# Optimization experiments

Hardware: AMD Instinct MI355X
Metric: run time of the kernel (lower is better)

The kernel has to match this reference:

```python
import jax, jax.numpy as jnp
import numpy as np

GRID_SIZE = 5
SPLINE_ORDER = 3
GRID_RANGE = (-0.2, 0.2)
N_TOK, IN_CH, OUT_CH = 8192, 1024, 1024
K_COEF = GRID_SIZE + SPLINE_ORDER  # 8 basis functions per feature


def _make_grid():
    lo, hi = GRID_RANGE
    h = (hi - lo) / GRID_SIZE
    # 12 knots, extended by spline_order on both sides
    return (jnp.arange(-SPLINE_ORDER, GRID_SIZE + SPLINE_ORDER + 1, dtype=jnp.float32) * h + lo)


def _b_splines(x, grid):
    # x: [N, in] -> bases: [N, in, K_COEF] via Cox-de Boor recursion
    xe = x[..., None]                      # [N, in, 1]
    G = grid.shape[0]                      # 12
    bases = ((xe >= grid[:-1]) & (xe < grid[1:])).astype(x.dtype)  # [N, in, G-1]
    for k in range(1, SPLINE_ORDER + 1):
        left = (xe - grid[: G - k - 1]) / (grid[k : G - 1] - grid[: G - k - 1]) * bases[..., :-1]
        right = (grid[k + 1 :] - xe) / (grid[k + 1 :] - grid[1 : G - k]) * bases[..., 1:]
        bases = left + right
    return bases                            # [N, in, 8]


def _kan_layer(x, base_w, spline_w, grid):
    # base_activation = Identity
    base_out = x @ base_w.T                               # [N, out]
    bases = _b_splines(x, grid)                           # [N, in, K]
    spline_out = jnp.einsum('nik,oik->no', bases, spline_w)
    return base_out + spline_out


def setup_inputs() -> dict:
    key = jax.random.key(0)
    k1, k2, k3, k4, k5 = jax.random.split(key, 5)
    lo, hi = GRID_RANGE
    x = jax.random.uniform(k1, (N_TOK, IN_CH), dtype=jnp.float32, minval=lo, maxval=hi)
    s = 0.1 / np.sqrt(IN_CH)
    return {
        'x': x,
        'base_w1': jax.random.normal(k2, (OUT_CH, IN_CH), dtype=jnp.float32) * s,
        'spline_w1': jax.random.normal(k3, (OUT_CH, IN_CH, K_COEF), dtype=jnp.float32) * s,
        'base_w2': jax.random.normal(k4, (OUT_CH, OUT_CH), dtype=jnp.float32) * s,
        'spline_w2': jax.random.normal(k5, (OUT_CH, OUT_CH, K_COEF), dtype=jnp.float32) * s,
    }


def reference(x, base_w1, spline_w1, base_w2, spline_w2):
    grid = _make_grid()
    x1 = _kan_layer(x, base_w1, spline_w1, grid)
    x2 = _kan_layer(x1, base_w2, spline_w2, grid)
    return x2
```

## Files before the change

kernel.cpp:

```cpp
#include <hip/hip_runtime.h>
#include <hip/hip_bf16.h>

typedef __attribute__((ext_vector_type(8))) short bf16x8;
typedef __attribute__((ext_vector_type(4))) float f32x4;
typedef __attribute__((ext_vector_type(4))) unsigned int u32x4;

#define KCAT 9216
#define NTOK 8192
#define CH   1024
#define KHALF 4608
#define BK   64
#define NT   (KHALF / BK)
#define NH   (2 * NT)

__device__ __forceinline__ unsigned short f2bf(float f) {
    union { float f; unsigned int u; } v; v.f = f;
    unsigned int r = v.u + 0x7fffu + ((v.u >> 16) & 1u);
    return (unsigned short)(r >> 16);
}

__device__ __forceinline__ void load16_to_lds(const void* gp, void* lp) {
    __builtin_amdgcn_global_load_lds(
        (__attribute__((address_space(1))) void*)(void*)gp,
        (__attribute__((address_space(3))) void*)lp,
        16, 0, 0);
}

__device__ __forceinline__ void bases8_cf(float x, unsigned int* w) {
    float p  = (x + 0.44f) * 12.5f;
    float mf = floorf(p);
    float u  = p - mf;
    int   m  = (int)mf;
    float v  = 1.0f - u;
    float u2 = u * u, u3 = u2 * u;
    float N0 = v * v * v * (1.0f / 6.0f);
    float N1 = 0.5f * u3 - u2 + (2.0f / 3.0f);
    float N3 = u3 * (1.0f / 6.0f);
    float N2 = 1.0f - N0 - N1 - N3;
    unsigned long long lo =
          (unsigned long long)f2bf(N0)
        | ((unsigned long long)f2bf(N1) << 16)
        | ((unsigned long long)f2bf(N2) << 32)
        | ((unsigned long long)f2bf(N3) << 48);
    lo = (m >= 0 && m <= 10) ? lo : 0ull;
    int sh  = (m - 3) * 16;
    int sh1 = sh - 64;
    unsigned long long d0 =
        (sh  >= 0) ? ((sh  < 64) ? (lo << sh)    : 0ull)
                   : ((-sh  < 64) ? (lo >> (-sh))  : 0ull);
    unsigned long long d1 =
        (sh1 >= 0) ? ((sh1 < 64) ? (lo << sh1)   : 0ull)
                   : ((-sh1 < 64) ? (lo >> (-sh1)) : 0ull);
    w[0] = (unsigned int)d0; w[1] = (unsigned int)(d0 >> 32);
    w[2] = (unsigned int)d1; w[3] = (unsigned int)(d1 >> 32);
}

__device__ __forceinline__ void conv_w_body(const float* __restrict__ BW,
                                            const float* __restrict__ SW,
                                            unsigned short* __restrict__ W, int o) {
    const float* bw = BW + (size_t)o * 1024;
    const float* sw = SW + (size_t)o * 8192;
    unsigned short* w = W + (size_t)o * KCAT;
    for (int c = threadIdx.x * 4; c < KCAT; c += 256 * 4) {
        const float* src = (c < 1024) ? (bw + c) : (sw + (c - 1024));
        float4 v = *(const float4*)src;
        unsigned short u[4] = { f2bf(v.x), f2bf(v.y), f2bf(v.z), f2bf(v.w) };
        *(unsigned long long*)(w + c) = *(unsigned long long*)u;
    }
}

__device__ __forceinline__ void basis_body(float x, unsigned short* __restrict__ A, int idx) {
    int n = idx >> 10, i = idx & 1023;
    size_t rowbase = (size_t)n * KCAT;
    A[rowbase + i] = f2bf(x);
    unsigned int w[4];
    bases8_cf(x, w);
    *(u32x4*)(A + rowbase + 1024 + (size_t)i * 8) = (u32x4){w[0], w[1], w[2], w[3]};
}

__global__ __launch_bounds__(256) void prep1(const float* __restrict__ BW1,
                                             const float* __restrict__ SW1,
                                             unsigned short* __restrict__ W,
                                             const float* __restrict__ X,
                                             unsigned short* __restrict__ A) {
    int b = blockIdx.x;
    if (b < 1024) { conv_w_body(BW1, SW1, W, b); return; }
    int bb = b - 1024;
    for (int idx = bb * 256 + threadIdx.x; idx < NTOK * CH; idx += 2048 * 256)
        basis_body(X[idx], A, idx);
}

__global__ __launch_bounds__(256) void mid2(const float* __restrict__ BW2,
                                            const float* __restrict__ SW2,
                                            unsigned short* __restrict__ W,
                                            const float* __restrict__ C0,
                                            const float* __restrict__ C1,
                                            unsigned short* __restrict__ A) {
    int b = blockIdx.x;
    if (b < 1024) { conv_w_body(BW2, SW2, W, b); return; }
    int bb = b - 1024;
    for (int idx = bb * 256 + threadIdx.x; idx < NTOK * CH; idx += 2048 * 256)
        basis_body(C0[idx] + C1[idx], A, idx);
}

__global__ __launch_bounds__(256) void add_out(const float* __restrict__ C0,
                                               const float* __restrict__ C1,
                                               float* __restrict__ out, int total4) {
    for (int i = blockIdx.x * 256 + threadIdx.x; i < total4; i += gridDim.x * 256) {
        float4 a = ((const float4*)C0)[i];
        float4 b = ((const float4*)C1)[i];
        float4 r = { a.x + b.x, a.y + b.y, a.z + b.z, a.w + b.w };
        ((float4*)out)[i] = r;
    }
}

__global__ __launch_bounds__(512, 2) void gemm256_splitk(const unsigned short* __restrict__ A,
                                                         const unsigned short* __restrict__ B,
                                                         float* __restrict__ C0,
                                                         float* __restrict__ C1) {
    __shared__ __align__(16) unsigned short As[4 * 256 * 32];
    __shared__ __align__(16) unsigned short Bs[4 * 256 * 32];
    const int tid  = threadIdx.x;
    const int lane = tid & 63;
    const int wid  = tid >> 6;
    const int wr = wid >> 2, wc = wid & 3;
    const int ln = lane & 15, q = lane >> 4;

    const int bid = blockIdx.x;
    const int xcd = bid & 7, ii = bid >> 3;
    const int kz = xcd & 1, chm = xcd >> 1;
    const int bm = chm * 8 + (ii & 7);
    const int bn = ii >> 3;

    const unsigned short* Ab = A + (size_t)(bm * 256) * KCAT + (size_t)kz * KHALF;
    const unsigned short* Bb = B + (size_t)(bn * 256) * KCAT + (size_t)kz * KHALF;
    float* C = (kz == 0) ? C0 : C1;

    f32x4 acc[8][4] = {};

    auto stageA2 = [&](int ts, int ks, int ds) {
#pragma unroll
        for (int part = 0; part < 2; ++part) {
            int c = part * 512 + tid;
            int r = c >> 2;
            int gslot = (c & 3) ^ ((r >> 1) & 3);
            size_t goff = (size_t)r * (KCAT * 2) + (size_t)ts * 128 + ks * 64 + gslot * 16;
            load16_to_lds((const char*)Ab + goff, (char*)As + (size_t)ds * 16384 + c * 16);
        }
    };
    auto stageB2 = [&](int ts, int ks, int ds) {
#pragma unroll
        for (int part = 0; part < 2; ++part) {
            int c = part * 512 + tid;
            int r = c >> 2;
            int gslot = (c & 3) ^ ((r >> 1) & 3);
            size_t goff = (size_t)r * (KCAT * 2) + (size_t)ts * 128 + ks * 64 + gslot * 16;
            load16_to_lds((const char*)Bb + goff, (char*)Bs + (size_t)ds * 16384 + c * 16);
        }
    };

    stageA2(0, 0, 0); stageB2(0, 0, 0);
    stageA2(0, 1, 1); stageB2(0, 1, 1);
    asm volatile("s_waitcnt vmcnt(4)" ::: "memory");
    __builtin_amdgcn_s_barrier();

    for (int t = 0; t < NT; ++t) {
#pragma unroll
        for (int kh = 0; kh < 2; ++kh) {
            const int j  = 2 * t + kh;
            const int sl = j & 3;
            const char* Ah = (const char*)As + sl * 16384;
            const char* Bh = (const char*)Bs + sl * 16384;
            const int jn = j + 2;
            const bool pf = jn < NH;
            const int ts = jn >> 1, ks = jn & 1, ds = jn & 3;
            bf16x8 bfr[4];
#pragma unroll
            for (int ph = 0; ph < 2; ++ph) {
                bf16x8 afr[4];
#pragma unroll
                for (int m = 0; m < 4; ++m) {
                    int row = wr * 128 + (ph * 4 + m) * 16 + ln;
                    afr[m] = *(const bf16x8*)(Ah + row * 64 + ((q ^ ((row >> 1) & 3)) * 16));
                }
                if (ph == 0) {
#pragma unroll
                    for (int nf = 0; nf < 4; ++nf) {
                        int row = wc * 64 + nf * 16 + ln;
                        bfr[nf] = *(const bf16x8*)(Bh + row * 64 + ((q ^ ((row >> 1) & 3)) * 16));
                    }
                }
                if (pf) { if (ph == 0) stageA2(ts, ks, ds); else stageB2(ts, ks, ds); }
                __builtin_amdgcn_s_barrier();
                asm volatile("s_waitcnt lgkmcnt(0)" ::: "memory");
                __builtin_amdgcn_sched_barrier(0);
                __builtin_amdgcn_s_setprio(1);
#pragma unroll
                for (int m = 0; m < 4; ++m)
#pragma unroll
                    for (int nf = 0; nf < 4; ++nf)
                        acc[ph * 4 + m][nf] = __builtin_amdgcn_mfma_f32_16x16x32_bf16(
                            afr[m], bfr[nf], acc[ph * 4 + m][nf], 0, 0, 0);
                __builtin_amdgcn_s_setprio(0);
                if (ph == 1) {
                    if (pf)               asm volatile("s_waitcnt vmcnt(4)" ::: "memory");
                    else if (j + 1 < NH)  asm volatile("s_waitcnt vmcnt(0)" ::: "memory");
                }
                __builtin_amdgcn_s_barrier();
            }
        }
    }

#pragma unroll
    for (int mf = 0; mf < 8; ++mf)
#pragma unroll
        for (int nf = 0; nf < 4; ++nf)
#pragma unroll
            for (int r = 0; r < 4; ++r) {
                int row = bm * 256 + wr * 128 + mf * 16 + q * 4 + r;
                int col = bn * 256 + wc * 64 + nf * 16 + ln;
                C[(size_t)row * CH + col] = acc[mf][nf][r];
            }
}

extern "C" void kernel_launch(void* const* d_in, const int* in_sizes, int n_in,
                              void* d_out, int out_size, void* d_ws, size_t ws_size,
                              hipStream_t stream) {
    const float* x   = (const float*)d_in[0];
    const float* bw1 = (const float*)d_in[1];
    const float* sw1 = (const float*)d_in[2];
    const float* bw2 = (const float*)d_in[3];
    const float* sw2 = (const float*)d_in[4];
    float* out = (float*)d_out;

    char* ws = (char*)d_ws;
    unsigned short* Abuf = (unsigned short*)ws;
    unsigned short* Wbuf = (unsigned short*)(ws + 150994944);
    float* C0 = (float*)(ws + 150994944 + 18874368);
    float* C1 = (float*)(ws + 150994944 + 18874368 + 33554432);

    prep1         <<<dim3(3072), dim3(256), 0, stream>>>(bw1, sw1, Wbuf, x, Abuf);
    gemm256_splitk<<<dim3(256), dim3(512), 0, stream>>>(Abuf, Wbuf, C0, C1);

    mid2          <<<dim3(3072), dim3(256), 0, stream>>>(bw2, sw2, Wbuf, C0, C1, Abuf);
    gemm256_splitk<<<dim3(256), dim3(512), 0, stream>>>(Abuf, Wbuf, C0, C1);
    add_out       <<<dim3(1024), dim3(256), 0, stream>>>(C0, C1, out, NTOK * CH / 4);
}
```

Baseline: 544.8 us.

## Load GEMM B fragments directly into registers and double-buffer only A in LDS

The split-K bf16 GEMM stops staging the B tile through LDS. Each wave now reads its B fragments straight from global memory into registers once per 64-wide K step. A is still staged through LDS, but as a full 256x64 tile with a two-buffer scheme, an 8-slot XOR swizzle, and prefetch spread across four MFMA phases. This halves LDS use and removes B's LDS writes and reads. In exchange, the B global load is issued only after a full vmcnt(0) drain at the end of each step, so its latency sits right before the next step's MFMAs, and waves sharing a column re-read the same B from cache.

```diff
diff --git a/kernel.cpp b/kernel.cpp
--- a/kernel.cpp
+++ b/kernel.cpp
@@ -11,7 +11,6 @@
 #define KHALF 4608
 #define BK   64
 #define NT   (KHALF / BK)
-#define NH   (2 * NT)
 
 __device__ __forceinline__ unsigned short f2bf(float f) {
     union { float f; unsigned int u; } v; v.f = f;
@@ -118,8 +117,7 @@
                                                          const unsigned short* __restrict__ B,
                                                          float* __restrict__ C0,
                                                          float* __restrict__ C1) {
-    __shared__ __align__(16) unsigned short As[4 * 256 * 32];
-    __shared__ __align__(16) unsigned short Bs[4 * 256 * 32];
+    __shared__ __align__(16) unsigned short As[2 * 256 * 64];
     const int tid  = threadIdx.x;
     const int lane = tid & 63;
     const int wid  = tid >> 6;
@@ -133,81 +131,71 @@
     const int bn = ii >> 3;
 
     const unsigned short* Ab = A + (size_t)(bm * 256) * KCAT + (size_t)kz * KHALF;
-    const unsigned short* Bb = B + (size_t)(bn * 256) * KCAT + (size_t)kz * KHALF;
+    const unsigned short* Bl = B + (size_t)(bn * 256 + wc * 64 + ln) * KCAT + (size_t)kz * KHALF;
     float* C = (kz == 0) ? C0 : C1;
 
     f32x4 acc[8][4] = {};
-
-    auto stageA2 = [&](int ts, int ks, int ds) {
-#pragma unroll
-        for (int part = 0; part < 2; ++part) {
-            int c = part * 512 + tid;
-            int r = c >> 2;
-            int gslot = (c & 3) ^ ((r >> 1) & 3);
-            size_t goff = (size_t)r * (KCAT * 2) + (size_t)ts * 128 + ks * 64 + gslot * 16;
-            load16_to_lds((const char*)Ab + goff, (char*)As + (size_t)ds * 16384 + c * 16);
-        }
+    bf16x8 bfr[4][2];
+
+    auto stageA = [&](int t, int buf, int part) {
+        int chunk = part * 512 + tid;
+        int r = chunk >> 3;
+        int slot = (chunk & 7) ^ (r & 7);
+        size_t goff = (size_t)r * (KCAT * 2) + (size_t)t * 128 + slot * 16;
+        load16_to_lds((const char*)Ab + goff, (char*)As + (size_t)buf * 32768 + chunk * 16);
     };
-    auto stageB2 = [&](int ts, int ks, int ds) {
-#pragma unroll
-        for (int part = 0; part < 2; ++part) {
-            int c = part * 512 + tid;
-            int r = c >> 2;
-            int gslot = (c & 3) ^ ((r >> 1) & 3);
-            size_t goff = (size_t)r * (KCAT * 2) + (size_t)ts * 128 + ks * 64 + gslot * 16;
-            load16_to_lds((const char*)Bb + goff, (char*)Bs + (size_t)ds * 16384 + c * 16);
-        }
+    auto loadB = [&](int t) {
+#pragma unroll
+        for (int nf = 0; nf < 4; ++nf)
+#pragma unroll
+            for (int kh = 0; kh < 2; ++kh)
+                bfr[nf][kh] = *(const bf16x8*)(Bl + (size_t)nf * 16 * KCAT
+                                                  + (size_t)t * BK + kh * 32 + q * 8);
     };
 
-    stageA2(0, 0, 0); stageB2(0, 0, 0);
-    stageA2(0, 1, 1); stageB2(0, 1, 1);
-    asm volatile("s_waitcnt vmcnt(4)" ::: "memory");
+    loadB(0);
+    stageA(0, 0, 0); stageA(0, 0, 1); stageA(0, 0, 2); stageA(0, 0, 3);
+    asm volatile("s_waitcnt vmcnt(0)" ::: "memory");
     __builtin_amdgcn_s_barrier();
 
     for (int t = 0; t < NT; ++t) {
-#pragma unroll
-        for (int kh = 0; kh < 2; ++kh) {
-            const int j  = 2 * t + kh;
-            const int sl = j & 3;
-            const char* Ah = (const char*)As + sl * 16384;
-            const char* Bh = (const char*)Bs + sl * 16384;
-            const int jn = j + 2;
-            const bool pf = jn < NH;
-            const int ts = jn >> 1, ks = jn & 1, ds = jn & 3;
-            bf16x8 bfr[4];
-#pragma unroll
-            for (int ph = 0; ph < 2; ++ph) {
-                bf16x8 afr[4];
-#pragma unroll
-                for (int m = 0; m < 4; ++m) {
-                    int row = wr * 128 + (ph * 4 + m) * 16 + ln;
-                    afr[m] = *(const bf16x8*)(Ah + row * 64 + ((q ^ ((row >> 1) & 3)) * 16));
+        const int c = t & 1;
+        const char* Ap = (const char*)As + c * 32768;
+        const bool pref = (t + 1 < NT);
+#pragma unroll
+        for (int p = 0; p < 4; ++p) {
+            bf16x8 afr[2][2];
+#pragma unroll
+            for (int m2 = 0; m2 < 2; ++m2)
+#pragma unroll
+                for (int kh = 0; kh < 2; ++kh) {
+                    int row = wr * 128 + (p * 2 + m2) * 16 + ln;
+                    int byte = row * 128 + ((kh * 64 + q * 16) ^ ((row & 7) * 16));
+                    afr[m2][kh] = *(const bf16x8*)(Ap + byte);
                 }
-                if (ph == 0) {
-#pragma unroll
-                    for (int nf = 0; nf < 4; ++nf) {
-                        int row = wc * 64 + nf * 16 + ln;
-                        bfr[nf] = *(const bf16x8*)(Bh + row * 64 + ((q ^ ((row >> 1) & 3)) * 16));
-                    }
-                }
-                if (pf) { if (ph == 0) stageA2(ts, ks, ds); else stageB2(ts, ks, ds); }
-                __builtin_amdgcn_s_barrier();
-                asm volatile("s_waitcnt lgkmcnt(0)" ::: "memory");
-                __builtin_amdgcn_sched_barrier(0);
-                __builtin_amdgcn_s_setprio(1);
-#pragma unroll
-                for (int m = 0; m < 4; ++m)
-#pragma unroll
-                    for (int nf = 0; nf < 4; ++nf)
-                        acc[ph * 4 + m][nf] = __builtin_amdgcn_mfma_f32_16x16x32_bf16(
-                            afr[m], bfr[nf], acc[ph * 4 + m][nf], 0, 0, 0);
-                __builtin_amdgcn_s_setprio(0);
-                if (ph == 1) {
-                    if (pf)               asm volatile("s_waitcnt vmcnt(4)" ::: "memory");
-                    else if (j + 1 < NH)  asm volatile("s_waitcnt vmcnt(0)" ::: "memory");
-                }
-                __builtin_amdgcn_s_barrier();
+            if (pref) {
+                if (p == 0)      { stageA(t + 1, c ^ 1, 0); stageA(t + 1, c ^ 1, 1); }
+                else if (p == 1) { stageA(t + 1, c ^ 1, 2); }
+                else if (p == 2) { stageA(t + 1, c ^ 1, 3); }
             }
+            __builtin_amdgcn_s_barrier();
+            asm volatile("s_waitcnt lgkmcnt(0)" ::: "memory");
+            __builtin_amdgcn_sched_barrier(0);
+            __builtin_amdgcn_s_setprio(1);
+#pragma unroll
+            for (int m2 = 0; m2 < 2; ++m2)
+#pragma unroll
+                for (int nf = 0; nf < 4; ++nf)
+#pragma unroll
+                    for (int kh = 0; kh < 2; ++kh)
+                        acc[p * 2 + m2][nf] = __builtin_amdgcn_mfma_f32_16x16x32_bf16(
+                            afr[m2][kh], bfr[nf][kh], acc[p * 2 + m2][nf], 0, 0, 0);
+            __builtin_amdgcn_s_setprio(0);
+            if (p == 3) {
+                asm volatile("s_waitcnt vmcnt(0)" ::: "memory");
+                if (pref) loadB(t + 1);
+            }
+            __builtin_amdgcn_s_barrier();
         }
     }
 
```

Result: slower. 676.9 us (+24.2%).

## Restructure GEMM main loop to one barrier per K32 tile with merged staging

Applied to the files above, without the earlier changes.

Replaces the two-phase per-half-tile loop (two barriers per K32 step, with A and B staged in separate phases) by a 4-deep ring indexed directly by tile. Each tile issues the A+B prefetch for tile+2 first, reads all 8 A and 4 B fragments, runs 32 MFMAs, then does a single vmcnt wait and one barrier. This is meant to halve barrier count and give the compiler freedom to overlap LDS reads with MFMAs. In exchange it drops the explicit lgkmcnt/sched_barrier control and raises fragment register pressure.

```diff
diff --git a/kernel.cpp b/kernel.cpp
--- a/kernel.cpp
+++ b/kernel.cpp
@@ -9,9 +9,7 @@
 #define NTOK 8192
 #define CH   1024
 #define KHALF 4608
-#define BK   64
-#define NT   (KHALF / BK)
-#define NH   (2 * NT)
+#define NT32 144
 
 __device__ __forceinline__ unsigned short f2bf(float f) {
     union { float f; unsigned int u; } v; v.f = f;
@@ -138,76 +136,54 @@
 
     f32x4 acc[8][4] = {};
 
-    auto stageA2 = [&](int ts, int ks, int ds) {
+    auto stage = [&](int tile, int ds) {
 #pragma unroll
         for (int part = 0; part < 2; ++part) {
             int c = part * 512 + tid;
             int r = c >> 2;
             int gslot = (c & 3) ^ ((r >> 1) & 3);
-            size_t goff = (size_t)r * (KCAT * 2) + (size_t)ts * 128 + ks * 64 + gslot * 16;
+            size_t goff = (size_t)r * (KCAT * 2) + (size_t)tile * 64 + gslot * 16;
             load16_to_lds((const char*)Ab + goff, (char*)As + (size_t)ds * 16384 + c * 16);
-        }
-    };
-    auto stageB2 = [&](int ts, int ks, int ds) {
-#pragma unroll
-        for (int part = 0; part < 2; ++part) {
-            int c = part * 512 + tid;
-            int r = c >> 2;
-            int gslot = (c & 3) ^ ((r >> 1) & 3);
-            size_t goff = (size_t)r * (KCAT * 2) + (size_t)ts * 128 + ks * 64 + gslot * 16;
             load16_to_lds((const char*)Bb + goff, (char*)Bs + (size_t)ds * 16384 + c * 16);
         }
     };
 
-    stageA2(0, 0, 0); stageB2(0, 0, 0);
-    stageA2(0, 1, 1); stageB2(0, 1, 1);
+    stage(0, 0);
+    stage(1, 1);
     asm volatile("s_waitcnt vmcnt(4)" ::: "memory");
     __builtin_amdgcn_s_barrier();
 
-    for (int t = 0; t < NT; ++t) {
-#pragma unroll
-        for (int kh = 0; kh < 2; ++kh) {
-            const int j  = 2 * t + kh;
-            const int sl = j & 3;
-            const char* Ah = (const char*)As + sl * 16384;
-            const char* Bh = (const char*)Bs + sl * 16384;
-            const int jn = j + 2;
-            const bool pf = jn < NH;
-            const int ts = jn >> 1, ks = jn & 1, ds = jn & 3;
-            bf16x8 bfr[4];
-#pragma unroll
-            for (int ph = 0; ph < 2; ++ph) {
-                bf16x8 afr[4];
-#pragma unroll
-                for (int m = 0; m < 4; ++m) {
-                    int row = wr * 128 + (ph * 4 + m) * 16 + ln;
-                    afr[m] = *(const bf16x8*)(Ah + row * 64 + ((q ^ ((row >> 1) & 3)) * 16));
-                }
-                if (ph == 0) {
-#pragma unroll
-                    for (int nf = 0; nf < 4; ++nf) {
-                        int row = wc * 64 + nf * 16 + ln;
-                        bfr[nf] = *(const bf16x8*)(Bh + row * 64 + ((q ^ ((row >> 1) & 3)) * 16));
-                    }
-                }
-                if (pf) { if (ph == 0) stageA2(ts, ks, ds); else stageB2(ts, ks, ds); }
-                __builtin_amdgcn_s_barrier();
-                asm volatile("s_waitcnt lgkmcnt(0)" ::: "memory");
-                __builtin_amdgcn_sched_barrier(0);
-                __builtin_amdgcn_s_setprio(1);
-#pragma unroll
-                for (int m = 0; m < 4; ++m)
-#pragma unroll
-                    for (int nf = 0; nf < 4; ++nf)
-                        acc[ph * 4 + m][nf] = __builtin_amdgcn_mfma_f32_16x16x32_bf16(
-                            afr[m], bfr[nf], acc[ph * 4 + m][nf], 0, 0, 0);
-                __builtin_amdgcn_s_setprio(0);
-                if (ph == 1) {
-                    if (pf)               asm volatile("s_waitcnt vmcnt(4)" ::: "memory");
-                    else if (j + 1 < NH)  asm volatile("s_waitcnt vmcnt(0)" ::: "memory");
-                }
-                __builtin_amdgcn_s_barrier();
+    for (int g = 0; g < NT32 / 4; ++g) {
+#pragma unroll
+        for (int u = 0; u < 4; ++u) {
+            const int tile = g * 4 + u;
+            const bool pf = (tile + 2) < NT32;
+            if (pf) stage(tile + 2, (u + 2) & 3);
+
+            const char* Ah = (const char*)As + u * 16384;
+            const char* Bh = (const char*)Bs + u * 16384;
+            bf16x8 afr[8], bfr[4];
+#pragma unroll
+            for (int f = 0; f < 8; ++f) {
+                int row = wr * 128 + f * 16 + ln;
+                afr[f] = *(const bf16x8*)(Ah + row * 64 + ((q ^ ((row >> 1) & 3)) * 16));
             }
+#pragma unroll
+            for (int nf = 0; nf < 4; ++nf) {
+                int row = wc * 64 + nf * 16 + ln;
+                bfr[nf] = *(const bf16x8*)(Bh + row * 64 + ((q ^ ((row >> 1) & 3)) * 16));
+            }
+            __builtin_amdgcn_s_setprio(1);
+#pragma unroll
+            for (int f = 0; f < 8; ++f)
+#pragma unroll
+                for (int nf = 0; nf < 4; ++nf)
+                    acc[f][nf] = __builtin_amdgcn_mfma_f32_16x16x32_bf16(
+                        afr[f], bfr[nf], acc[f][nf], 0, 0, 0);
+            __builtin_amdgcn_s_setprio(0);
+            if (pf) asm volatile("s_waitcnt vmcnt(4)" ::: "memory");
+            else    asm volatile("s_waitcnt vmcnt(0)" ::: "memory");
+            __builtin_amdgcn_s_barrier();
         }
     }
 
```

After: 488.8 us. 1.11x faster.
